# Optimization experiments

Hardware: AMD Instinct MI355X
Metric: run time of the kernel (lower is better)

Reference implementation:

```python
import jax, jax.numpy as jnp
import numpy as np

B = 16384        # batch
N_IN = 784       # n_input_neurons
D = 64           # n_neurons_per_hidd_bank
N_LAYERS = 6     # layers of hidden banks
BANKS = 6        # banks per layer (n_hidd_banks = 36)
N_OUT = 10       # n_output_neurons
EPS = 1e-5       # BatchNorm1d eps


def setup_inputs() -> dict:
    key = jax.random.key(0)
    ks = jax.random.split(key, 8)
    x = jax.random.normal(ks[0], (B, N_IN), dtype=jnp.float32)
    gamma_in = jnp.ones((N_IN,), jnp.float32)
    beta_in = jnp.zeros((N_IN,), jnp.float32)
    # input2hidden Linear(N_IN -> D) for each of the 6 input banks (layer 0)
    W_in = jax.random.normal(ks[1], (BANKS, D, N_IN), jnp.float32) * 0.03
    b_in = jax.random.normal(ks[2], (BANKS, D), jnp.float32) * 0.03
    # per-edge gate Linear(D -> 1, no bias) and data Linear(D -> D, bias)
    # indexed [layer, source_bank, target_bank, ...]
    Wg = jax.random.normal(ks[3], (N_LAYERS - 1, BANKS, BANKS, D), jnp.float32) * 0.1
    Wd = jax.random.normal(ks[4], (N_LAYERS - 1, BANKS, BANKS, D, D), jnp.float32) * 0.1
    bd = jax.random.normal(ks[5], (N_LAYERS - 1, BANKS, BANKS, D), jnp.float32) * 0.1
    # per-bank BatchNorm1d(D) affine params, [layer, bank, D]
    gamma_h = jnp.ones((N_LAYERS, BANKS, D), jnp.float32)
    beta_h = jnp.zeros((N_LAYERS, BANKS, D), jnp.float32)
    # hidden2output Linear(D -> N_OUT, no bias) for the 6 output banks (last layer)
    W_out = jax.random.normal(ks[6], (BANKS, N_OUT, D), jnp.float32) * 0.1
    return dict(x=x, gamma_in=gamma_in, beta_in=beta_in, W_in=W_in, b_in=b_in,
                Wg=Wg, Wd=Wd, bd=bd, gamma_h=gamma_h, beta_h=beta_h, W_out=W_out)


def _bn(x, g, b):
    # training-mode BatchNorm1d: normalize over batch axis 0, biased variance
    mu = jnp.mean(x, axis=0)
    var = jnp.mean((x - mu) ** 2, axis=0)
    return g * (x - mu) * jax.lax.rsqrt(var + EPS) + b


def reference(x, gamma_in, beta_in, W_in, b_in, Wg, Wd, bd, gamma_h, beta_h, W_out):
    xb = _bn(x, gamma_in, beta_in)                                  # [B, N_IN]
    # input banks: relu(input2hidden(x)); then (as targets with no sources)
    # relu (idempotent) + BatchNorm, matching the target loop in torch
    acts = jax.nn.relu(jnp.einsum('bn,kdn->bkd', xb, W_in) + b_in)  # [B, 6, D]
    acts = _bn(jax.nn.relu(acts), gamma_h[0], beta_h[0])
    total_gate = jnp.zeros((x.shape[0], 1), x.dtype)                # sum of [B,1] gate acts
    for l in range(N_LAYERS - 1):
        # gate: hardtanh(Linear(D->1), 0, 1) per edge (s,t)
        gate = jnp.clip(jnp.einsum('bsd,std->bst', acts, Wg[l]), 0.0, 1.0)  # [B,6,6]
        # data: Linear(D->D) per edge
        data = jnp.einsum('bsd,sted->bste', acts, Wd[l]) + bd[l]            # [B,6,6,D]
        pre = jnp.einsum('bst,bste->bte', gate, data)                       # sum over sources
        total_gate = total_gate + jnp.sum(gate, axis=(1, 2))[:, None]
        acts = _bn(jax.nn.relu(pre), gamma_h[l + 1], beta_h[l + 1])         # [B,6,D]
    # output banks = last layer banks; sum of Linear(D->N_OUT, no bias)
    output = jnp.einsum('bkd,kod->bo', acts, W_out)                         # [B, N_OUT]
    return output, total_gate
```

## Files before the change

kernel.cpp:

```cpp
#include <hip/hip_runtime.h>
#include <hip/hip_bf16.h>

#define BATCH   16384
#define NIN     784
#define NH      384
#define NLAYERS 6
#define NOUT    10
#define EPS_BN  1e-5f
#define LOSCALE 2048.0f
#define LOINV   (1.0f/2048.0f)
#define NPART   128
#define PSTRIDE 1024

typedef __attribute__((ext_vector_type(8))) _Float16 f16x8;
typedef __attribute__((ext_vector_type(4))) _Float16 f16x4;
typedef __attribute__((ext_vector_type(4))) float f32x4;

__global__ __launch_bounds__(256) void stats_partial(
        const float* __restrict__ src, int C, int applyRelu,
        float* __restrict__ psum, float* __restrict__ psq) {
    int c = blockIdx.x * 256 + threadIdx.x;
    if (c >= C) return;
    int r0 = blockIdx.y * (BATCH / NPART);
    float s = 0.f, q = 0.f;
    for (int r = r0; r < r0 + BATCH / NPART; ++r) {
        float v = src[(size_t)r * C + c];
        if (applyRelu) v = fmaxf(v, 0.f);
        s += v; q += v * v;
    }
    psum[blockIdx.y * PSTRIDE + c] = s;
    psq [blockIdx.y * PSTRIDE + c] = q;
}

__global__ __launch_bounds__(256) void stats_finalize(
        const float* __restrict__ psum, const float* __restrict__ psq, int C,
        const float* __restrict__ gamma, const float* __restrict__ beta,
        float* __restrict__ a_out, float* __restrict__ c_out) {
    int c = blockIdx.x * 256 + threadIdx.x;
    if (c >= C) return;
    float s = 0.f, q = 0.f;
    for (int i = 0; i < NPART; ++i) { s += psum[i * PSTRIDE + c]; q += psq[i * PSTRIDE + c]; }
    const float invB = 1.f / (float)BATCH;
    float mu  = s * invB;
    float var = q * invB - mu * mu;
    float rs  = rsqrtf(var + EPS_BN);
    float g   = gamma[c];
    a_out[c] = g * rs;
    c_out[c] = beta[c] - g * mu * rs;
}

__global__ __launch_bounds__(256) void scale_win_hl(
        const float* __restrict__ W_in, const float* __restrict__ a,
        _Float16* __restrict__ whi, _Float16* __restrict__ wlo) {
    int i = blockIdx.x * 256 + threadIdx.x;
    if (i >= NH * NIN / 4) return;
    int n = (i * 4) % NIN;
    float4 wv = ((const float4*)W_in)[i];
    float v[4] = { wv.x * a[n], wv.y * a[n + 1], wv.z * a[n + 2], wv.w * a[n + 3] };
    f16x4 h4, l4;
    #pragma unroll
    for (int j = 0; j < 4; ++j) {
        _Float16 h = (_Float16)v[j];
        h4[j] = h;
        l4[j] = (_Float16)((v[j] - (float)h) * LOSCALE);
    }
    *(f16x4*)(whi + (size_t)i * 4) = h4;
    *(f16x4*)(wlo + (size_t)i * 4) = l4;
}

__global__ __launch_bounds__(256) void conv_hl(
        const float* __restrict__ src, _Float16* __restrict__ hi,
        _Float16* __restrict__ lo, int n4) {
    int i = blockIdx.x * 256 + threadIdx.x;
    if (i >= n4) return;
    float4 wv = ((const float4*)src)[i];
    float v[4] = { wv.x, wv.y, wv.z, wv.w };
    f16x4 h4, l4;
    #pragma unroll
    for (int j = 0; j < 4; ++j) {
        _Float16 h = (_Float16)v[j];
        h4[j] = h;
        l4[j] = (_Float16)((v[j] - (float)h) * LOSCALE);
    }
    *(f16x4*)(hi + (size_t)i * 4) = h4;
    *(f16x4*)(lo + (size_t)i * 4) = l4;
}

__global__ __launch_bounds__(256) void prep_wg(
        const float* __restrict__ Wg, _Float16* __restrict__ hi,
        _Float16* __restrict__ lo) {
    int idx = blockIdx.x * 256 + threadIdx.x;
    if (idx >= 5 * 48 * 384) return;
    int l = idx / (48 * 384);
    int r = idx % (48 * 384);
    int st = r / 384, k = r % 384;
    float v = 0.f;
    if (st < 36 && (k >> 6) == st / 6)
        v = Wg[l * 36 * 64 + st * 64 + (k & 63)];
    _Float16 h = (_Float16)v;
    hi[idx] = h;
    lo[idx] = (_Float16)((v - (float)h) * LOSCALE);
}

__global__ __launch_bounds__(256) void prep_wout(
        const float* __restrict__ W_out, _Float16* __restrict__ hi,
        _Float16* __restrict__ lo) {
    int idx = blockIdx.x * 256 + threadIdx.x;
    if (idx >= 16 * 384) return;
    int o = idx / 384, k = idx % 384;
    float v = 0.f;
    if (o < NOUT) v = W_out[((k >> 6) * NOUT + o) * 64 + (k & 63)];
    _Float16 h = (_Float16)v;
    hi[idx] = h;
    lo[idx] = (_Float16)((v - (float)h) * LOSCALE);
}

__global__ __launch_bounds__(64) void bias_in(
        const float* __restrict__ W_in, const float* __restrict__ b_in,
        const float* __restrict__ cvec, float* __restrict__ bp) {
    int j = blockIdx.x;
    int lane = threadIdx.x;
    float s = 0.f;
    for (int n = lane; n < NIN; n += 64) s += cvec[n] * W_in[j * NIN + n];
    #pragma unroll
    for (int m = 1; m < 64; m <<= 1) s += __shfl_xor(s, m, 64);
    if (lane == 0) bp[j] = b_in[j] + s;
}

__global__ __launch_bounds__(256, 2) void gemm_in_mfma(
        const float* __restrict__ X, const _Float16* __restrict__ Wphi,
        const _Float16* __restrict__ Wplo, const float* __restrict__ bp,
        float* __restrict__ pre) {
    int tid = threadIdx.x;
    int w = tid >> 6, l = tid & 63, lr = l & 15, lq = l >> 4;
    int b0 = blockIdx.x * 128 + w * 32;
    int n0 = blockIdx.y * 96;
    const float* xrow0 = X + (size_t)(b0 + lr) * NIN;
    const float* xrow1 = X + (size_t)(b0 + 16 + lr) * NIN;
    f32x4 acc[6][2], acr[6][2];
    #pragma unroll
    for (int ct = 0; ct < 6; ++ct)
        #pragma unroll
        for (int bt = 0; bt < 2; ++bt)
            #pragma unroll
            for (int r = 0; r < 4; ++r) { acc[ct][bt][r] = 0.f; acr[ct][bt][r] = 0.f; }
    for (int kc = 0; kc < 24; ++kc) {
        int k0 = kc * 32 + lq * 8;
        f16x8 ahi[2], alo[2];
        {
            float4 x0 = *(const float4*)(xrow0 + k0);
            float4 x1 = *(const float4*)(xrow0 + k0 + 4);
            float xv[8] = { x0.x, x0.y, x0.z, x0.w, x1.x, x1.y, x1.z, x1.w };
            #pragma unroll
            for (int j = 0; j < 8; ++j) {
                _Float16 h = (_Float16)xv[j];
                ahi[0][j] = h;
                alo[0][j] = (_Float16)((xv[j] - (float)h) * LOSCALE);
            }
            float4 y0 = *(const float4*)(xrow1 + k0);
            float4 y1 = *(const float4*)(xrow1 + k0 + 4);
            float yv[8] = { y0.x, y0.y, y0.z, y0.w, y1.x, y1.y, y1.z, y1.w };
            #pragma unroll
            for (int j = 0; j < 8; ++j) {
                _Float16 h = (_Float16)yv[j];
                ahi[1][j] = h;
                alo[1][j] = (_Float16)((yv[j] - (float)h) * LOSCALE);
            }
        }
        #pragma unroll
        for (int ct = 0; ct < 6; ++ct) {
            size_t off = (size_t)(n0 + ct * 16 + lr) * NIN + k0;
            f16x8 bhi = *(const f16x8*)(Wphi + off);
            f16x8 blo = *(const f16x8*)(Wplo + off);
            #pragma unroll
            for (int bt = 0; bt < 2; ++bt) {
                acc[ct][bt] = __builtin_amdgcn_mfma_f32_16x16x32_f16(ahi[bt], bhi, acc[ct][bt], 0, 0, 0);
                acr[ct][bt] = __builtin_amdgcn_mfma_f32_16x16x32_f16(ahi[bt], blo, acr[ct][bt], 0, 0, 0);
                acr[ct][bt] = __builtin_amdgcn_mfma_f32_16x16x32_f16(alo[bt], bhi, acr[ct][bt], 0, 0, 0);
            }
        }
    }
    {
        f16x8 ahi[2], alo[2];
        #pragma unroll
        for (int bt = 0; bt < 2; ++bt)
            #pragma unroll
            for (int j = 0; j < 8; ++j) { ahi[bt][j] = (_Float16)0.f; alo[bt][j] = (_Float16)0.f; }
        if (lq < 2) {
            const float* xr[2] = { xrow0, xrow1 };
            #pragma unroll
            for (int bt = 0; bt < 2; ++bt) {
                float4 x0 = *(const float4*)(xr[bt] + 768 + lq * 8);
                float4 x1 = *(const float4*)(xr[bt] + 768 + lq * 8 + 4);
                float xv[8] = { x0.x, x0.y, x0.z, x0.w, x1.x, x1.y, x1.z, x1.w };
                #pragma unroll
                for (int j = 0; j < 8; ++j) {
                    _Float16 h = (_Float16)xv[j];
                    ahi[bt][j] = h;
                    alo[bt][j] = (_Float16)((xv[j] - (float)h) * LOSCALE);
                }
            }
        }
        #pragma unroll
        for (int ct = 0; ct < 6; ++ct) {
            f16x8 bhi, blo;
            #pragma unroll
            for (int j = 0; j < 8; ++j) { bhi[j] = (_Float16)0.f; blo[j] = (_Float16)0.f; }
            if (lq < 2) {
                size_t off = (size_t)(n0 + ct * 16 + lr) * NIN + 768 + lq * 8;
                bhi = *(const f16x8*)(Wphi + off);
                blo = *(const f16x8*)(Wplo + off);
            }
            #pragma unroll
            for (int bt = 0; bt < 2; ++bt) {
                acc[ct][bt] = __builtin_amdgcn_mfma_f32_16x16x32_f16(ahi[bt], bhi, acc[ct][bt], 0, 0, 0);
                acr[ct][bt] = __builtin_amdgcn_mfma_f32_16x16x32_f16(ahi[bt], blo, acr[ct][bt], 0, 0, 0);
                acr[ct][bt] = __builtin_amdgcn_mfma_f32_16x16x32_f16(alo[bt], bhi, acr[ct][bt], 0, 0, 0);
            }
        }
    }
    #pragma unroll
    for (int ct = 0; ct < 6; ++ct) {
        int n = n0 + ct * 16 + lr;
        float bias = bp[n];
        #pragma unroll
        for (int bt = 0; bt < 2; ++bt) {
            int brow = b0 + bt * 16 + lq * 4;
            #pragma unroll
            for (int r = 0; r < 4; ++r)
                pre[(size_t)(brow + r) * NH + n] = acc[ct][bt][r] + LOINV * acr[ct][bt][r] + bias;
        }
    }
}

__global__ __launch_bounds__(256) void norm_hl(
        const float* __restrict__ pre, const float* __restrict__ a,
        const float* __restrict__ c, _Float16* __restrict__ hi,
        _Float16* __restrict__ lo) {
    int idx = blockIdx.x * 256 + threadIdx.x;
    int j = (idx * 8) % NH;
    float4 v0 = ((const float4*)pre)[idx * 2];
    float4 v1 = ((const float4*)pre)[idx * 2 + 1];
    float y[8] = {
        a[j+0] * fmaxf(v0.x, 0.f) + c[j+0], a[j+1] * fmaxf(v0.y, 0.f) + c[j+1],
        a[j+2] * fmaxf(v0.z, 0.f) + c[j+2], a[j+3] * fmaxf(v0.w, 0.f) + c[j+3],
        a[j+4] * fmaxf(v1.x, 0.f) + c[j+4], a[j+5] * fmaxf(v1.y, 0.f) + c[j+5],
        a[j+6] * fmaxf(v1.z, 0.f) + c[j+6], a[j+7] * fmaxf(v1.w, 0.f) + c[j+7] };
    f16x8 h8, l8;
    #pragma unroll
    for (int jj = 0; jj < 8; ++jj) {
        _Float16 h = (_Float16)y[jj];
        h8[jj] = h;
        l8[jj] = (_Float16)((y[jj] - (float)h) * LOSCALE);
    }
    *(f16x8*)(hi + (size_t)idx * 8) = h8;
    *(f16x8*)(lo + (size_t)idx * 8) = l8;
}

__global__ __launch_bounds__(256, 2) void gate_mfma(
        const _Float16* __restrict__ aHi, const _Float16* __restrict__ aLo,
        const _Float16* __restrict__ WgHi, const _Float16* __restrict__ WgLo,
        float* __restrict__ gateT, float* __restrict__ tg, int firstLayer) {
    int tid = threadIdx.x;
    int w = tid >> 6, l = tid & 63, lr = l & 15, lq = l >> 4;
    int b = blockIdx.x * 64 + w * 16 + lr;
    const _Float16* arowH = aHi + (size_t)b * NH;
    const _Float16* arowL = aLo + (size_t)b * NH;
    f32x4 acc[3], acr[3];
    #pragma unroll
    for (int rt = 0; rt < 3; ++rt)
        #pragma unroll
        for (int r = 0; r < 4; ++r) { acc[rt][r] = 0.f; acr[rt][r] = 0.f; }
    #pragma unroll
    for (int kc = 0; kc < 12; ++kc) {
        int k0 = kc * 32 + lq * 8;
        f16x8 bhi = *(const f16x8*)(arowH + k0);
        f16x8 blo = *(const f16x8*)(arowL + k0);
        #pragma unroll
        for (int rt = 0; rt < 3; ++rt) {
            size_t off = (size_t)(rt * 16 + lr) * NH + k0;
            f16x8 ahi = *(const f16x8*)(WgHi + off);
            f16x8 alo = *(const f16x8*)(WgLo + off);
            acc[rt] = __builtin_amdgcn_mfma_f32_16x16x32_f16(ahi, bhi, acc[rt], 0, 0, 0);
            acr[rt] = __builtin_amdgcn_mfma_f32_16x16x32_f16(ahi, blo, acr[rt], 0, 0, 0);
            acr[rt] = __builtin_amdgcn_mfma_f32_16x16x32_f16(alo, bhi, acr[rt], 0, 0, 0);
        }
    }
    float gsum = 0.f;
    #pragma unroll
    for (int rt = 0; rt < 3; ++rt)
        #pragma unroll
        for (int r = 0; r < 4; ++r) {
            int st = rt * 16 + lq * 4 + r;
            if (st < 36) {
                float p = acc[rt][r] + LOINV * acr[rt][r];
                float g = fminf(fmaxf(p, 0.f), 1.f);
                gateT[(size_t)st * BATCH + b] = g;
                gsum += g;
            }
        }
    gsum += __shfl_xor(gsum, 16, 64);
    gsum += __shfl_xor(gsum, 32, 64);
    if (lq == 0) tg[b] = (firstLayer ? 0.f : tg[b]) + gsum;
}

__global__ __launch_bounds__(256, 2) void layer_data_mfma(
        const _Float16* __restrict__ aHi, const _Float16* __restrict__ aLo,
        const float* __restrict__ gateT, const _Float16* __restrict__ Wdhi,
        const _Float16* __restrict__ Wdlo, const float* __restrict__ bd_l,
        float* __restrict__ pre) {
    int tid = threadIdx.x;
    int w = tid >> 6, l = tid & 63, lr = l & 15, lq = l >> 4;
    int b0 = blockIdx.x * 64;
    int t0 = blockIdx.y * 3;
    int e0 = w * 16;
    f32x4 acc[3][4];
    #pragma unroll
    for (int t = 0; t < 3; ++t)
        #pragma unroll
        for (int ct = 0; ct < 4; ++ct)
            #pragma unroll
            for (int r = 0; r < 4; ++r) acc[t][ct][r] = 0.f;
    for (int s = 0; s < 6; ++s) {
        f16x8 bhi[4][2], blo[4][2];
        #pragma unroll
        for (int ct = 0; ct < 4; ++ct) {
            size_t arow = (size_t)(b0 + ct * 16 + lr) * NH + s * 64 + lq * 8;
            #pragma unroll
            for (int ks = 0; ks < 2; ++ks) {
                bhi[ct][ks] = *(const f16x8*)(aHi + arow + ks * 32);
                blo[ct][ks] = *(const f16x8*)(aLo + arow + ks * 32);
            }
        }
        #pragma unroll
        for (int tt = 0; tt < 3; ++tt) {
            int t = t0 + tt;
            float g[4];
            #pragma unroll
            for (int ct = 0; ct < 4; ++ct)
                g[ct] = gateT[(size_t)(s * 6 + t) * BATCH + b0 + ct * 16 + lr];
            size_t wb = ((size_t)(s * 6 + t) * 64 + e0 + lr) * 64 + lq * 8;
            f16x8 ah0 = *(const f16x8*)(Wdhi + wb);
            f16x8 ah1 = *(const f16x8*)(Wdhi + wb + 32);
            f16x8 al0 = *(const f16x8*)(Wdlo + wb);
            f16x8 al1 = *(const f16x8*)(Wdlo + wb + 32);
            float bdv[4];
            #pragma unroll
            for (int r = 0; r < 4; ++r)
                bdv[r] = bd_l[(s * 6 + t) * 64 + e0 + lq * 4 + r];
            #pragma unroll
            for (int ct = 0; ct < 4; ++ct) {
                f32x4 ph, pc;
                #pragma unroll
                for (int r = 0; r < 4; ++r) { ph[r] = 0.f; pc[r] = 0.f; }
                ph = __builtin_amdgcn_mfma_f32_16x16x32_f16(ah0, bhi[ct][0], ph, 0, 0, 0);
                ph = __builtin_amdgcn_mfma_f32_16x16x32_f16(ah1, bhi[ct][1], ph, 0, 0, 0);
                pc = __builtin_amdgcn_mfma_f32_16x16x32_f16(ah0, blo[ct][0], pc, 0, 0, 0);
                pc = __builtin_amdgcn_mfma_f32_16x16x32_f16(ah1, blo[ct][1], pc, 0, 0, 0);
                pc = __builtin_amdgcn_mfma_f32_16x16x32_f16(al0, bhi[ct][0], pc, 0, 0, 0);
                pc = __builtin_amdgcn_mfma_f32_16x16x32_f16(al1, bhi[ct][1], pc, 0, 0, 0);
                #pragma unroll
                for (int r = 0; r < 4; ++r)
                    acc[tt][ct][r] += g[ct] * (ph[r] + LOINV * pc[r] + bdv[r]);
            }
        }
    }
    #pragma unroll
    for (int tt = 0; tt < 3; ++tt)
        #pragma unroll
        for (int ct = 0; ct < 4; ++ct)
            #pragma unroll
            for (int r = 0; r < 4; ++r)
                pre[(size_t)(b0 + ct * 16 + lr) * NH + (t0 + tt) * 64 + e0 + lq * 4 + r]
                    = acc[tt][ct][r];
}

__global__ __launch_bounds__(256, 2) void out_mfma(
        const _Float16* __restrict__ aHi, const _Float16* __restrict__ aLo,
        const _Float16* __restrict__ OutHi, const _Float16* __restrict__ OutLo,
        const float* __restrict__ tg, float* __restrict__ dout) {
    int tid = threadIdx.x;
    int w = tid >> 6, l = tid & 63, lr = l & 15, lq = l >> 4;
    int b = blockIdx.x * 64 + w * 16 + lr;
    const _Float16* arowH = aHi + (size_t)b * NH;
    const _Float16* arowL = aLo + (size_t)b * NH;
    f32x4 acc, acr;
    #pragma unroll
    for (int r = 0; r < 4; ++r) { acc[r] = 0.f; acr[r] = 0.f; }
    #pragma unroll
    for (int kc = 0; kc < 12; ++kc) {
        int k0 = kc * 32 + lq * 8;
        f16x8 bhi = *(const f16x8*)(arowH + k0);
        f16x8 blo = *(const f16x8*)(arowL + k0);
        size_t off = (size_t)lr * NH + k0;
        f16x8 ahi = *(const f16x8*)(OutHi + off);
        f16x8 alo = *(const f16x8*)(OutLo + off);
        acc = __builtin_amdgcn_mfma_f32_16x16x32_f16(ahi, bhi, acc, 0, 0, 0);
        acr = __builtin_amdgcn_mfma_f32_16x16x32_f16(ahi, blo, acr, 0, 0, 0);
        acr = __builtin_amdgcn_mfma_f32_16x16x32_f16(alo, bhi, acr, 0, 0, 0);
    }
    #pragma unroll
    for (int r = 0; r < 4; ++r) {
        int o = lq * 4 + r;
        if (o < NOUT)
            dout[(size_t)b * NOUT + o] = acc[r] + LOINV * acr[r];
    }
    if (lq == 0) dout[(size_t)BATCH * NOUT + b] = tg[b];
}

extern "C" void kernel_launch(void* const* d_in, const int* in_sizes, int n_in,
                              void* d_out, int out_size, void* d_ws, size_t ws_size,
                              hipStream_t stream) {
    const float* x        = (const float*)d_in[0];
    const float* gamma_in = (const float*)d_in[1];
    const float* beta_in  = (const float*)d_in[2];
    const float* W_in     = (const float*)d_in[3];
    const float* b_in     = (const float*)d_in[4];
    const float* Wg       = (const float*)d_in[5];
    const float* Wd       = (const float*)d_in[6];
    const float* bd       = (const float*)d_in[7];
    const float* gamma_h  = (const float*)d_in[8];
    const float* beta_h   = (const float*)d_in[9];
    const float* W_out    = (const float*)d_in[10];
    float* dout = (float*)d_out;
    float* ws = (float*)d_ws;

    float* psum  = ws;
    float* psq   = ws + 131072;
    float* avec  = ws + 262144;
    float* cvec  = ws + 263168;
    float* bp    = ws + 264192;
    float* pre   = ws + 265216;
    _Float16* actsHi = (_Float16*)(ws + 6556672);
    _Float16* actsLo = (_Float16*)(ws + 9702400);
    float* gateT = ws + 12848128;
    float* tg    = ws + 13437952;
    _Float16* WpHi = (_Float16*)(ws + 13454336);
    _Float16* WpLo = (_Float16*)(ws + 13604864);
    _Float16* WdHiAll = (_Float16*)(ws + 13755392);
    _Float16* WdLoAll = (_Float16*)(ws + 14124032);
    _Float16* WgHiAll = (_Float16*)(ws + 14492672);
    _Float16* WgLoAll = (_Float16*)(ws + 14538752);
    _Float16* OutHi   = (_Float16*)(ws + 14584832);
    _Float16* OutLo   = (_Float16*)(ws + 14587904);

    dim3 blk(256);

    stats_partial<<<dim3(4, NPART), blk, 0, stream>>>(x, NIN, 0, psum, psq);
    stats_finalize<<<dim3(4), blk, 0, stream>>>(psum, psq, NIN, gamma_in, beta_in, avec, cvec);
    scale_win_hl<<<dim3((NH * NIN / 4 + 255) / 256), blk, 0, stream>>>(W_in, avec, WpHi, WpLo);
    bias_in<<<dim3(NH), dim3(64), 0, stream>>>(W_in, b_in, cvec, bp);
    conv_hl<<<dim3((5 * 36 * 4096 / 4 + 255) / 256), blk, 0, stream>>>(
            Wd, WdHiAll, WdLoAll, 5 * 36 * 4096 / 4);
    prep_wg<<<dim3((5 * 48 * 384 + 255) / 256), blk, 0, stream>>>(Wg, WgHiAll, WgLoAll);
    prep_wout<<<dim3((16 * 384 + 255) / 256), blk, 0, stream>>>(W_out, OutHi, OutLo);

    gemm_in_mfma<<<dim3(BATCH / 128, 4), blk, 0, stream>>>(x, WpHi, WpLo, bp, pre);

    for (int j = 0; j < NLAYERS; ++j) {
        stats_partial<<<dim3(2, NPART), blk, 0, stream>>>(pre, NH, 1, psum, psq);
        stats_finalize<<<dim3(2), blk, 0, stream>>>(psum, psq, NH,
                gamma_h + j * NH, beta_h + j * NH, avec, cvec);
        norm_hl<<<dim3(BATCH * NH / 8 / 256), blk, 0, stream>>>(pre, avec, cvec, actsHi, actsLo);
        if (j < NLAYERS - 1) {
            int l = j;
            gate_mfma<<<dim3(BATCH / 64), blk, 0, stream>>>(
                    actsHi, actsLo, WgHiAll + (size_t)l * 48 * 384,
                    WgLoAll + (size_t)l * 48 * 384, gateT, tg, l == 0);
            layer_data_mfma<<<dim3(BATCH / 64, 2), blk, 0, stream>>>(
                    actsHi, actsLo, gateT, WdHiAll + (size_t)l * 36 * 4096,
                    WdLoAll + (size_t)l * 36 * 4096, bd + (size_t)l * 36 * 64, pre);
        }
    }

    out_mfma<<<dim3(BATCH / 64), blk, 0, stream>>>(actsHi, actsLo, OutHi, OutLo, tg, dout);
}
```

Measured before the change: 620.6 us.

## Fuse ReLU and BatchNorm partial statistics into GEMM epilogues, drop stats pass

The input GEMM and the per-layer data kernel now apply ReLU in their epilogues and write per-block column sum and sum-of-squares partials directly. This removes the separate stats_partial pass over the full pre-activation buffer at every layer. The finalize step now reduces 512 or 256 partials instead of 128, and the workspace is re-laid out to fit them. The data kernel's target split changes from 2×3 to 3×2 targets per block to lower register pressure, and the bias load is vectorised.

```diff
diff --git a/kernel.cpp b/kernel.cpp
--- a/kernel.cpp
+++ b/kernel.cpp
@@ -9,7 +9,7 @@
 #define EPS_BN  1e-5f
 #define LOSCALE 2048.0f
 #define LOINV   (1.0f/2048.0f)
-#define NPART   128
+#define NPART_X 128
 #define PSTRIDE 1024
 
 typedef __attribute__((ext_vector_type(8))) _Float16 f16x8;
@@ -17,15 +17,14 @@
 typedef __attribute__((ext_vector_type(4))) float f32x4;
 
 __global__ __launch_bounds__(256) void stats_partial(
-        const float* __restrict__ src, int C, int applyRelu,
+        const float* __restrict__ src, int C,
         float* __restrict__ psum, float* __restrict__ psq) {
     int c = blockIdx.x * 256 + threadIdx.x;
     if (c >= C) return;
-    int r0 = blockIdx.y * (BATCH / NPART);
+    int r0 = blockIdx.y * (BATCH / NPART_X);
     float s = 0.f, q = 0.f;
-    for (int r = r0; r < r0 + BATCH / NPART; ++r) {
+    for (int r = r0; r < r0 + BATCH / NPART_X; ++r) {
         float v = src[(size_t)r * C + c];
-        if (applyRelu) v = fmaxf(v, 0.f);
         s += v; q += v * v;
     }
     psum[blockIdx.y * PSTRIDE + c] = s;
@@ -34,12 +33,12 @@
 
 __global__ __launch_bounds__(256) void stats_finalize(
         const float* __restrict__ psum, const float* __restrict__ psq, int C,
-        const float* __restrict__ gamma, const float* __restrict__ beta,
+        int npart, const float* __restrict__ gamma, const float* __restrict__ beta,
         float* __restrict__ a_out, float* __restrict__ c_out) {
     int c = blockIdx.x * 256 + threadIdx.x;
     if (c >= C) return;
     float s = 0.f, q = 0.f;
-    for (int i = 0; i < NPART; ++i) { s += psum[i * PSTRIDE + c]; q += psq[i * PSTRIDE + c]; }
+    for (int i = 0; i < npart; ++i) { s += psum[i * PSTRIDE + c]; q += psq[i * PSTRIDE + c]; }
     const float invB = 1.f / (float)BATCH;
     float mu  = s * invB;
     float var = q * invB - mu * mu;
@@ -130,7 +129,7 @@
 __global__ __launch_bounds__(256, 2) void gemm_in_mfma(
         const float* __restrict__ X, const _Float16* __restrict__ Wphi,
         const _Float16* __restrict__ Wplo, const float* __restrict__ bp,
-        float* __restrict__ pre) {
+        float* __restrict__ pre, float* __restrict__ psum, float* __restrict__ psq) {
     int tid = threadIdx.x;
     int w = tid >> 6, l = tid & 63, lr = l & 15, lq = l >> 4;
     int b0 = blockIdx.x * 128 + w * 32;
@@ -219,16 +218,32 @@
             }
         }
     }
+    float ssum[6], ssq[6];
     #pragma unroll
     for (int ct = 0; ct < 6; ++ct) {
         int n = n0 + ct * 16 + lr;
         float bias = bp[n];
+        float s = 0.f, q = 0.f;
         #pragma unroll
         for (int bt = 0; bt < 2; ++bt) {
             int brow = b0 + bt * 16 + lq * 4;
             #pragma unroll
-            for (int r = 0; r < 4; ++r)
-                pre[(size_t)(brow + r) * NH + n] = acc[ct][bt][r] + LOINV * acr[ct][bt][r] + bias;
+            for (int r = 0; r < 4; ++r) {
+                float v = fmaxf(acc[ct][bt][r] + LOINV * acr[ct][bt][r] + bias, 0.f);
+                pre[(size_t)(brow + r) * NH + n] = v;
+                s += v; q += v * v;
+            }
+        }
+        s += __shfl_xor(s, 16, 64); s += __shfl_xor(s, 32, 64);
+        q += __shfl_xor(q, 16, 64); q += __shfl_xor(q, 32, 64);
+        ssum[ct] = s; ssq[ct] = q;
+    }
+    if (l < 16) {
+        int prow = blockIdx.x * 4 + w;
+        #pragma unroll
+        for (int ct = 0; ct < 6; ++ct) {
+            psum[prow * PSTRIDE + n0 + ct * 16 + l] = ssum[ct];
+            psq [prow * PSTRIDE + n0 + ct * 16 + l] = ssq[ct];
         }
     }
 }
@@ -308,15 +323,15 @@
         const _Float16* __restrict__ aHi, const _Float16* __restrict__ aLo,
         const float* __restrict__ gateT, const _Float16* __restrict__ Wdhi,
         const _Float16* __restrict__ Wdlo, const float* __restrict__ bd_l,
-        float* __restrict__ pre) {
+        float* __restrict__ pre, float* __restrict__ psum, float* __restrict__ psq) {
     int tid = threadIdx.x;
     int w = tid >> 6, l = tid & 63, lr = l & 15, lq = l >> 4;
     int b0 = blockIdx.x * 64;
-    int t0 = blockIdx.y * 3;
+    int t0 = blockIdx.y * 2;
     int e0 = w * 16;
-    f32x4 acc[3][4];
-    #pragma unroll
-    for (int t = 0; t < 3; ++t)
+    f32x4 acc[2][4];
+    #pragma unroll
+    for (int t = 0; t < 2; ++t)
         #pragma unroll
         for (int ct = 0; ct < 4; ++ct)
             #pragma unroll
@@ -333,7 +348,7 @@
             }
         }
         #pragma unroll
-        for (int tt = 0; tt < 3; ++tt) {
+        for (int tt = 0; tt < 2; ++tt) {
             int t = t0 + tt;
             float g[4];
             #pragma unroll
@@ -344,10 +359,7 @@
             f16x8 ah1 = *(const f16x8*)(Wdhi + wb + 32);
             f16x8 al0 = *(const f16x8*)(Wdlo + wb);
             f16x8 al1 = *(const f16x8*)(Wdlo + wb + 32);
-            float bdv[4];
-            #pragma unroll
-            for (int r = 0; r < 4; ++r)
-                bdv[r] = bd_l[(s * 6 + t) * 64 + e0 + lq * 4 + r];
+            float4 bdv = *(const float4*)(bd_l + (s * 6 + t) * 64 + e0 + lq * 4);
             #pragma unroll
             for (int ct = 0; ct < 4; ++ct) {
                 f32x4 ph, pc;
@@ -359,20 +371,35 @@
                 pc = __builtin_amdgcn_mfma_f32_16x16x32_f16(ah1, blo[ct][1], pc, 0, 0, 0);
                 pc = __builtin_amdgcn_mfma_f32_16x16x32_f16(al0, bhi[ct][0], pc, 0, 0, 0);
                 pc = __builtin_amdgcn_mfma_f32_16x16x32_f16(al1, bhi[ct][1], pc, 0, 0, 0);
+                float bd4[4] = { bdv.x, bdv.y, bdv.z, bdv.w };
                 #pragma unroll
                 for (int r = 0; r < 4; ++r)
-                    acc[tt][ct][r] += g[ct] * (ph[r] + LOINV * pc[r] + bdv[r]);
-            }
-        }
-    }
-    #pragma unroll
-    for (int tt = 0; tt < 3; ++tt)
-        #pragma unroll
-        for (int ct = 0; ct < 4; ++ct)
-            #pragma unroll
-            for (int r = 0; r < 4; ++r)
-                pre[(size_t)(b0 + ct * 16 + lr) * NH + (t0 + tt) * 64 + e0 + lq * 4 + r]
-                    = acc[tt][ct][r];
+                    acc[tt][ct][r] += g[ct] * (ph[r] + LOINV * pc[r] + bd4[r]);
+            }
+        }
+    }
+    #pragma unroll
+    for (int tt = 0; tt < 2; ++tt) {
+        #pragma unroll
+        for (int r = 0; r < 4; ++r) {
+            float s = 0.f, q = 0.f;
+            #pragma unroll
+            for (int ct = 0; ct < 4; ++ct) {
+                float v = fmaxf(acc[tt][ct][r], 0.f);
+                pre[(size_t)(b0 + ct * 16 + lr) * NH + (t0 + tt) * 64 + e0 + lq * 4 + r] = v;
+                s += v; q += v * v;
+            }
+            s += __shfl_xor(s, 1, 64); s += __shfl_xor(s, 2, 64);
+            s += __shfl_xor(s, 4, 64); s += __shfl_xor(s, 8, 64);
+            q += __shfl_xor(q, 1, 64); q += __shfl_xor(q, 2, 64);
+            q += __shfl_xor(q, 4, 64); q += __shfl_xor(q, 8, 64);
+            if (lr == 0) {
+                int col = (t0 + tt) * 64 + e0 + lq * 4 + r;
+                psum[blockIdx.x * PSTRIDE + col] = s;
+                psq [blockIdx.x * PSTRIDE + col] = q;
+            }
+        }
+    }
 }
 
 __global__ __launch_bounds__(256, 2) void out_mfma(
@@ -426,28 +453,29 @@
     float* ws = (float*)d_ws;
 
     float* psum  = ws;
-    float* psq   = ws + 131072;
-    float* avec  = ws + 262144;
-    float* cvec  = ws + 263168;
-    float* bp    = ws + 264192;
-    float* pre   = ws + 265216;
-    _Float16* actsHi = (_Float16*)(ws + 6556672);
-    _Float16* actsLo = (_Float16*)(ws + 9702400);
-    float* gateT = ws + 12848128;
-    float* tg    = ws + 13437952;
-    _Float16* WpHi = (_Float16*)(ws + 13454336);
-    _Float16* WpLo = (_Float16*)(ws + 13604864);
-    _Float16* WdHiAll = (_Float16*)(ws + 13755392);
-    _Float16* WdLoAll = (_Float16*)(ws + 14124032);
-    _Float16* WgHiAll = (_Float16*)(ws + 14492672);
-    _Float16* WgLoAll = (_Float16*)(ws + 14538752);
-    _Float16* OutHi   = (_Float16*)(ws + 14584832);
-    _Float16* OutLo   = (_Float16*)(ws + 14587904);
+    float* psq   = ws + 524288;
+    float* avec  = ws + 1048576;
+    float* cvec  = ws + 1049600;
+    float* bp    = ws + 1050624;
+    float* pre   = ws + 1051648;
+    _Float16* actsHi = (_Float16*)(ws + 7343104);
+    _Float16* actsLo = (_Float16*)(ws + 10488832);
+    float* gateT = ws + 13634560;
+    float* tg    = ws + 14224384;
+    _Float16* WpHi = (_Float16*)(ws + 14240768);
+    _Float16* WpLo = (_Float16*)(ws + 14391296);
+    _Float16* WdHiAll = (_Float16*)(ws + 14541824);
+    _Float16* WdLoAll = (_Float16*)(ws + 14910464);
+    _Float16* WgHiAll = (_Float16*)(ws + 15279104);
+    _Float16* WgLoAll = (_Float16*)(ws + 15325184);
+    _Float16* OutHi   = (_Float16*)(ws + 15371264);
+    _Float16* OutLo   = (_Float16*)(ws + 15374336);
 
     dim3 blk(256);
 
-    stats_partial<<<dim3(4, NPART), blk, 0, stream>>>(x, NIN, 0, psum, psq);
-    stats_finalize<<<dim3(4), blk, 0, stream>>>(psum, psq, NIN, gamma_in, beta_in, avec, cvec);
+    stats_partial<<<dim3(4, NPART_X), blk, 0, stream>>>(x, NIN, psum, psq);
+    stats_finalize<<<dim3(4), blk, 0, stream>>>(psum, psq, NIN, NPART_X,
+            gamma_in, beta_in, avec, cvec);
     scale_win_hl<<<dim3((NH * NIN / 4 + 255) / 256), blk, 0, stream>>>(W_in, avec, WpHi, WpLo);
     bias_in<<<dim3(NH), dim3(64), 0, stream>>>(W_in, b_in, cvec, bp);
     conv_hl<<<dim3((5 * 36 * 4096 / 4 + 255) / 256), blk, 0, stream>>>(
@@ -455,11 +483,11 @@
     prep_wg<<<dim3((5 * 48 * 384 + 255) / 256), blk, 0, stream>>>(Wg, WgHiAll, WgLoAll);
     prep_wout<<<dim3((16 * 384 + 255) / 256), blk, 0, stream>>>(W_out, OutHi, OutLo);
 
-    gemm_in_mfma<<<dim3(BATCH / 128, 4), blk, 0, stream>>>(x, WpHi, WpLo, bp, pre);
+    gemm_in_mfma<<<dim3(BATCH / 128, 4), blk, 0, stream>>>(x, WpHi, WpLo, bp, pre, psum, psq);
 
     for (int j = 0; j < NLAYERS; ++j) {
-        stats_partial<<<dim3(2, NPART), blk, 0, stream>>>(pre, NH, 1, psum, psq);
-        stats_finalize<<<dim3(2), blk, 0, stream>>>(psum, psq, NH,
+        int npart = (j == 0) ? 512 : 256;
+        stats_finalize<<<dim3(2), blk, 0, stream>>>(psum, psq, NH, npart,
                 gamma_h + j * NH, beta_h + j * NH, avec, cvec);
         norm_hl<<<dim3(BATCH * NH / 8 / 256), blk, 0, stream>>>(pre, avec, cvec, actsHi, actsLo);
         if (j < NLAYERS - 1) {
@@ -467,9 +495,10 @@
             gate_mfma<<<dim3(BATCH / 64), blk, 0, stream>>>(
                     actsHi, actsLo, WgHiAll + (size_t)l * 48 * 384,
                     WgLoAll + (size_t)l * 48 * 384, gateT, tg, l == 0);
-            layer_data_mfma<<<dim3(BATCH / 64, 2), blk, 0, stream>>>(
+            layer_data_mfma<<<dim3(BATCH / 64, 3), blk, 0, stream>>>(
                     actsHi, actsLo, gateT, WdHiAll + (size_t)l * 36 * 4096,
-                    WdLoAll + (size_t)l * 36 * 4096, bd + (size_t)l * 36 * 64, pre);
+                    WdLoAll + (size_t)l * 36 * 4096, bd + (size_t)l * 36 * 64,
+                    pre, psum, psq);
         }
     }
 
```

Measured after the change: 1.675 ms. 2.7x slower.

## Fuse BN normalize/split into gate kernel and retile data kernel over targets

Applied to the files above, without the earlier changes.

For layers that feed a gate, the normalize-and-split-to-hi/lo step moves into the gate MFMA kernel. That kernel now reads fp32 pre-activations, applies the BN affine and ReLU, writes the hi/lo fp16 activations and uses them directly, which removes one launch and one read of the activation buffer per layer. Separately, layer_data_mfma now handles 2 targets per block instead of 3, with a grid of 3 in y, which raises block count and cuts accumulator registers. The cost is that each data block reloads the source activation tiles more times, and the last layer still uses the standalone normalize kernel.

```diff
diff --git a/kernel.cpp b/kernel.cpp
--- a/kernel.cpp
+++ b/kernel.cpp
@@ -257,15 +257,16 @@
     *(f16x8*)(lo + (size_t)idx * 8) = l8;
 }
 
-__global__ __launch_bounds__(256, 2) void gate_mfma(
-        const _Float16* __restrict__ aHi, const _Float16* __restrict__ aLo,
-        const _Float16* __restrict__ WgHi, const _Float16* __restrict__ WgLo,
-        float* __restrict__ gateT, float* __restrict__ tg, int firstLayer) {
+__global__ __launch_bounds__(256, 2) void normgate_mfma(
+        const float* __restrict__ pre, const float* __restrict__ a,
+        const float* __restrict__ c, const _Float16* __restrict__ WgHi,
+        const _Float16* __restrict__ WgLo, _Float16* __restrict__ aHi,
+        _Float16* __restrict__ aLo, float* __restrict__ gateT,
+        float* __restrict__ tg, int firstLayer) {
     int tid = threadIdx.x;
     int w = tid >> 6, l = tid & 63, lr = l & 15, lq = l >> 4;
     int b = blockIdx.x * 64 + w * 16 + lr;
-    const _Float16* arowH = aHi + (size_t)b * NH;
-    const _Float16* arowL = aLo + (size_t)b * NH;
+    const float* prow = pre + (size_t)b * NH;
     f32x4 acc[3], acr[3];
     #pragma unroll
     for (int rt = 0; rt < 3; ++rt)
@@ -274,16 +275,34 @@
     #pragma unroll
     for (int kc = 0; kc < 12; ++kc) {
         int k0 = kc * 32 + lq * 8;
-        f16x8 bhi = *(const f16x8*)(arowH + k0);
-        f16x8 blo = *(const f16x8*)(arowL + k0);
+        float4 v0 = *(const float4*)(prow + k0);
+        float4 v1 = *(const float4*)(prow + k0 + 4);
+        float4 a0 = *(const float4*)(a + k0);
+        float4 a1 = *(const float4*)(a + k0 + 4);
+        float4 c0 = *(const float4*)(c + k0);
+        float4 c1 = *(const float4*)(c + k0 + 4);
+        float y[8] = {
+            a0.x * fmaxf(v0.x, 0.f) + c0.x, a0.y * fmaxf(v0.y, 0.f) + c0.y,
+            a0.z * fmaxf(v0.z, 0.f) + c0.z, a0.w * fmaxf(v0.w, 0.f) + c0.w,
+            a1.x * fmaxf(v1.x, 0.f) + c1.x, a1.y * fmaxf(v1.y, 0.f) + c1.y,
+            a1.z * fmaxf(v1.z, 0.f) + c1.z, a1.w * fmaxf(v1.w, 0.f) + c1.w };
+        f16x8 bhi, blo;
+        #pragma unroll
+        for (int j = 0; j < 8; ++j) {
+            _Float16 h = (_Float16)y[j];
+            bhi[j] = h;
+            blo[j] = (_Float16)((y[j] - (float)h) * LOSCALE);
+        }
+        *(f16x8*)(aHi + (size_t)b * NH + k0) = bhi;
+        *(f16x8*)(aLo + (size_t)b * NH + k0) = blo;
         #pragma unroll
         for (int rt = 0; rt < 3; ++rt) {
             size_t off = (size_t)(rt * 16 + lr) * NH + k0;
-            f16x8 ahi = *(const f16x8*)(WgHi + off);
-            f16x8 alo = *(const f16x8*)(WgLo + off);
-            acc[rt] = __builtin_amdgcn_mfma_f32_16x16x32_f16(ahi, bhi, acc[rt], 0, 0, 0);
-            acr[rt] = __builtin_amdgcn_mfma_f32_16x16x32_f16(ahi, blo, acr[rt], 0, 0, 0);
-            acr[rt] = __builtin_amdgcn_mfma_f32_16x16x32_f16(alo, bhi, acr[rt], 0, 0, 0);
+            f16x8 whi = *(const f16x8*)(WgHi + off);
+            f16x8 wlo = *(const f16x8*)(WgLo + off);
+            acc[rt] = __builtin_amdgcn_mfma_f32_16x16x32_f16(whi, bhi, acc[rt], 0, 0, 0);
+            acr[rt] = __builtin_amdgcn_mfma_f32_16x16x32_f16(whi, blo, acr[rt], 0, 0, 0);
+            acr[rt] = __builtin_amdgcn_mfma_f32_16x16x32_f16(wlo, bhi, acr[rt], 0, 0, 0);
         }
     }
     float gsum = 0.f;
@@ -312,11 +331,11 @@
     int tid = threadIdx.x;
     int w = tid >> 6, l = tid & 63, lr = l & 15, lq = l >> 4;
     int b0 = blockIdx.x * 64;
-    int t0 = blockIdx.y * 3;
+    int t0 = blockIdx.y * 2;
     int e0 = w * 16;
-    f32x4 acc[3][4];
-    #pragma unroll
-    for (int t = 0; t < 3; ++t)
+    f32x4 acc[2][4];
+    #pragma unroll
+    for (int t = 0; t < 2; ++t)
         #pragma unroll
         for (int ct = 0; ct < 4; ++ct)
             #pragma unroll
@@ -333,7 +352,7 @@
             }
         }
         #pragma unroll
-        for (int tt = 0; tt < 3; ++tt) {
+        for (int tt = 0; tt < 2; ++tt) {
             int t = t0 + tt;
             float g[4];
             #pragma unroll
@@ -366,7 +385,7 @@
         }
     }
     #pragma unroll
-    for (int tt = 0; tt < 3; ++tt)
+    for (int tt = 0; tt < 2; ++tt)
         #pragma unroll
         for (int ct = 0; ct < 4; ++ct)
             #pragma unroll
@@ -461,15 +480,17 @@
         stats_partial<<<dim3(2, NPART), blk, 0, stream>>>(pre, NH, 1, psum, psq);
         stats_finalize<<<dim3(2), blk, 0, stream>>>(psum, psq, NH,
                 gamma_h + j * NH, beta_h + j * NH, avec, cvec);
-        norm_hl<<<dim3(BATCH * NH / 8 / 256), blk, 0, stream>>>(pre, avec, cvec, actsHi, actsLo);
         if (j < NLAYERS - 1) {
             int l = j;
-            gate_mfma<<<dim3(BATCH / 64), blk, 0, stream>>>(
-                    actsHi, actsLo, WgHiAll + (size_t)l * 48 * 384,
-                    WgLoAll + (size_t)l * 48 * 384, gateT, tg, l == 0);
-            layer_data_mfma<<<dim3(BATCH / 64, 2), blk, 0, stream>>>(
+            normgate_mfma<<<dim3(BATCH / 64), blk, 0, stream>>>(
+                    pre, avec, cvec, WgHiAll + (size_t)l * 48 * 384,
+                    WgLoAll + (size_t)l * 48 * 384, actsHi, actsLo, gateT, tg, l == 0);
+            layer_data_mfma<<<dim3(BATCH / 64, 3), blk, 0, stream>>>(
                     actsHi, actsLo, gateT, WdHiAll + (size_t)l * 36 * 4096,
                     WdLoAll + (size_t)l * 36 * 4096, bd + (size_t)l * 36 * 64, pre);
+        } else {
+            norm_hl<<<dim3(BATCH * NH / 8 / 256), blk, 0, stream>>>(
+                    pre, avec, cvec, actsHi, actsLo);
         }
     }
 
```

Result: slower. 850.5 us (+37.1%).
